# Optimization experiments

Hardware: AMD Instinct MI355X
Metric: run time of the kernel (lower is better)

## Reference

```python
import jax, jax.numpy as jnp
import numpy as np
from jax import lax

D = 768          # embed_dim
H = 12           # n_heads
DEPTH = 2
T = 6            # n_timepoints
PS = 7           # patch_size
IMG = (56, 49, 49)
GRID = (8, 7, 7)
NPATCH = 392     # prod(GRID), must be even for the sinusoidal PE
SEQ = T * NPATCH # 2352 space-time tokens
MLP_H = 3072     # int(768 * 4.0)
B = 2
RRELU_MLP = 0.4        # eval-mode RReLU(0.1, 0.7) slope
RRELU_HEAD = 11.0/48.0 # eval-mode RReLU(1/8, 1/3) slope


def _ln(x, g, b, eps=1e-6):
    m = x.mean(-1, keepdims=True)
    v = ((x - m) ** 2).mean(-1, keepdims=True)
    return (x - m) / jnp.sqrt(v + eps) * g + b


def _pos_enc(t, d):
    pos = np.arange(t, dtype=np.float32)[:, None]
    div = 1.0 / 10000.0 ** (np.arange(0, d, 2, dtype=np.float32) / d)
    pe = np.zeros((t, d), np.float32)
    pe[:, 0::2] = np.sin(pos * div)
    pe[:, 1::2] = np.cos(pos * div)
    return jnp.asarray(pe)


def _convT_dw(x, w, bias, stride, dilation):
    # depthwise ConvTranspose3d(C, C, k, stride, dilation, groups=C); w: (C,1,k,k,k)
    C = x.shape[1]
    k = w.shape[-1]
    wf = jnp.flip(w, axis=(2, 3, 4))
    pad = (k - 1) * dilation
    y = lax.conv_general_dilated(
        x, wf, window_strides=(1, 1, 1), padding=[(pad, pad)] * 3,
        lhs_dilation=(stride,) * 3, rhs_dilation=(dilation,) * 3,
        dimension_numbers=('NCDHW', 'OIDHW', 'NCDHW'), feature_group_count=C)
    return y + bias[None, :, None, None, None]


def _nearest(x, size):
    # torch F.interpolate(mode='nearest'): src = floor(dst * in/out)
    for ax, s in zip((2, 3, 4), size):
        idx = (jnp.arange(s) * (x.shape[ax] / s)).astype(jnp.int32)
        x = jnp.take(x, idx, axis=ax)
    return x


def setup_inputs() -> dict:
    key = jax.random.key(0)
    ks = iter(jax.random.split(key, 64))
    def rn(shape, s=0.02):
        return jax.random.normal(next(ks), shape, jnp.float32) * s
    inp = {}
    inp['x'] = jax.random.normal(next(ks), (B, 1, T) + IMG, jnp.float32)
    inp['pconv_w'] = rn((D, 1, PS, PS, PS)); inp['pconv_b'] = rn((D,))
    inp['pos_embed'] = rn((1, SEQ, D))
    inp['ln1_g'] = jnp.ones((DEPTH, D)); inp['ln1_b'] = jnp.zeros((DEPTH, D))
    inp['qkv_w'] = rn((DEPTH, 3 * D, D)); inp['qkv_b'] = rn((DEPTH, 3 * D))
    inp['proj_w'] = rn((DEPTH, D, D)); inp['proj_b'] = rn((DEPTH, D))
    inp['ln2_g'] = jnp.ones((DEPTH, D)); inp['ln2_b'] = jnp.zeros((DEPTH, D))
    inp['fc1_w'] = rn((DEPTH, MLP_H, D)); inp['fc1_b'] = rn((DEPTH, MLP_H))
    inp['fc2_w'] = rn((DEPTH, D, MLP_H)); inp['fc2_b'] = rn((DEPTH, D))
    inp['normf_g'] = jnp.ones((D,)); inp['normf_b'] = jnp.zeros((D,))
    inp['dfc_w'] = rn((1, D)); inp['dfc_b'] = rn((1,))
    inp['up1_w'] = rn((T, 1, 7, 7, 7)); inp['up1_b'] = rn((T,))
    inp['up2_w'] = rn((T, 1, 5, 5, 5)); inp['up2_b'] = rn((T,))
    inp['up3_w'] = rn((T, 1, 9, 9, 9)); inp['up3_b'] = rn((T,))
    inp['hconv_w'] = rn((T, 1, 1, 1, 1)); inp['hconv_b'] = rn((T,))
    return inp


def reference(x, pconv_w, pconv_b, pos_embed, ln1_g, ln1_b, qkv_w, qkv_b,
              proj_w, proj_b, ln2_g, ln2_b, fc1_w, fc1_b, fc2_w, fc2_b,
              normf_g, normf_b, dfc_w, dfc_b, up1_w, up1_b, up2_w, up2_b,
              up3_w, up3_b, hconv_w, hconv_b):
    b = x.shape[0]
    hd = D // H
    scale = hd ** -0.5
    # fold time into batch, patch-embed each 3D frame
    xt = x.transpose(0, 2, 1, 3, 4, 5).reshape(b * T, 1, *IMG)
    y = lax.conv_general_dilated(
        xt, pconv_w, (PS, PS, PS), 'VALID',
        dimension_numbers=('NCDHW', 'OIDHW', 'NCDHW'))
    y = y + pconv_b[None, :, None, None, None]
    tok = y.reshape(b * T, D, NPATCH).transpose(0, 2, 1).reshape(b, SEQ, D)
    tok = tok + pos_embed
    for i in range(DEPTH):
        h = _ln(tok, ln1_g[i], ln1_b[i])
        qkv = (h @ qkv_w[i].T + qkv_b[i]).reshape(b, SEQ, 3, H, hd)
        qkv = qkv.transpose(2, 0, 3, 1, 4)  # (3,b,H,SEQ,hd)
        q, k, v = qkv[0], qkv[1], qkv[2]
        attn = jax.nn.softmax(jnp.einsum('bhnd,bhmd->bhnm', q, k) * scale, axis=-1)
        o = jnp.einsum('bhnm,bhmd->bhnd', attn, v)
        o = o.transpose(0, 2, 1, 3).reshape(b, SEQ, D)
        tok = tok + (o @ proj_w[i].T + proj_b[i])
        h = _ln(tok, ln2_g[i], ln2_b[i])
        h = h @ fc1_w[i].T + fc1_b[i]
        h = jnp.where(h >= 0, h, RRELU_MLP * h)
        tok = tok + (h @ fc2_w[i].T + fc2_b[i])
    tok = _ln(tok, normf_g, normf_b)
    z = tok.reshape(b, T, NPATCH, D)
    # --- DecoderHead ---
    z = (z @ dfc_w.T + dfc_b)[..., 0]           # (b,T,NPATCH)
    z = z - z.mean(axis=1, keepdims=True)       # subtract time mean
    z = z + _pos_enc(T, NPATCH)
    z = z.reshape(b, T, *GRID)                  # (b,T,8,7,7)
    z = _convT_dw(z, up1_w, up1_b, 1, 1)        # -> (b,T,14,13,13)
    z = _convT_dw(z, up2_w, up2_b, 2, 1)        # -> (b,T,31,29,29)
    z = _convT_dw(z, up3_w, up3_b, 1, 2)        # -> (b,T,47,45,45)
    z = _nearest(z, IMG)                        # -> (b,T,56,49,49)
    z = z * hconv_w[:, 0, 0, 0, 0][None, :, None, None, None] \
        + hconv_b[None, :, None, None, None]
    z = jnp.where(z >= 0, z, RRELU_HEAD * z)
    return z[:, None].transpose(0, 1, 3, 4, 5, 2)  # (b,1,56,49,49,T)
```

## Files before the change

### kernel.cpp

```cpp
#include <hip/hip_runtime.h>


#define AS1 __attribute__((address_space(1)))
#define AS3 __attribute__((address_space(3)))

using bf16 = __bf16;
typedef __bf16 bf16x8 __attribute__((ext_vector_type(8)));
typedef float  f32x4  __attribute__((ext_vector_type(4)));

#define CDIV(a, b) (((a) + (b) - 1) / (b))

__device__ __forceinline__ void gll16(const void* g, void* l) {
  __builtin_amdgcn_global_load_lds((AS1 void*)(void*)g, (AS3 void*)l, 16, 0, 0);
}

template <int SH>
__device__ __forceinline__ float rorf(float x) {
  int i = __builtin_amdgcn_update_dpp(0, __builtin_bit_cast(int, x),
                                      0x120 + SH, 0xF, 0xF, false);
  return __builtin_bit_cast(float, i);
}
__device__ __forceinline__ float rowsum16(float v) {
  v += rorf<1>(v); v += rorf<2>(v); v += rorf<4>(v); v += rorf<8>(v);
  return v;
}

__global__ __launch_bounds__(256) void gemm_bt(
    const bf16* __restrict__ A, const bf16* __restrict__ B,
    float* Cf, bf16* Cb, const float* __restrict__ bias,
    const float* addp, int addmod, int rrelu,
    int M, int N, int K, int lda, int ldb, int ldc,
    long long sA, long long sB, long long sC, int ksplit,
    bf16* __restrict__ Qo, bf16* __restrict__ Ko, bf16* __restrict__ Vo) {
  __shared__ __align__(16) bf16 As[128 * 32];
  __shared__ __align__(16) bf16 Bs[128 * 32];
  const int tid  = threadIdx.x;
  const int lane = tid & 63;
  const int wave = tid >> 6;
  const int wm = wave & 1;
  const int wn = wave >> 1;
  const int q  = lane >> 4;
  const int r  = lane & 15;
  const int tm0 = blockIdx.x * 128;
  const int tn0 = blockIdx.y * 128;
  const int z   = blockIdx.z;

  const bf16* Ab = A + (ksplit > 1 ? 0 : (size_t)z * (size_t)sA);
  const bf16* Bb = B + (ksplit > 1 ? 0 : (size_t)z * (size_t)sB);
  int kb = 0, ke = K;
  if (ksplit > 1) {
    const int kc = ((K / ksplit + 31) / 32) * 32;
    kb = z * kc;
    ke = min(kb + kc, K);
  }

  const int arow0 = min(tm0 + (tid >> 2), M - 1);
  const int arow1 = min(tm0 + (tid >> 2) + 64, M - 1);
  const int brow0 = min(tn0 + (tid >> 2), N - 1);
  const int brow1 = min(tn0 + (tid >> 2) + 64, N - 1);
  const int kcol  = (tid & 3) * 8;
  const bf16* ap0 = Ab + (size_t)arow0 * lda + kcol;
  const bf16* ap1 = Ab + (size_t)arow1 * lda + kcol;
  const bf16* bp0 = Bb + (size_t)brow0 * ldb + kcol;
  const bf16* bp1 = Bb + (size_t)brow1 * ldb + kcol;
  bf16* asw0 = &As[(wave * 64) * 8];
  bf16* asw1 = &As[(256 + wave * 64) * 8];
  bf16* bsw0 = &Bs[(wave * 64) * 8];
  bf16* bsw1 = &Bs[(256 + wave * 64) * 8];

  f32x4 acc[4][4];
#pragma unroll
  for (int mi = 0; mi < 4; ++mi)
#pragma unroll
    for (int ni = 0; ni < 4; ++ni) acc[mi][ni] = (f32x4){0.f, 0.f, 0.f, 0.f};

  for (int k0 = kb; k0 < ke; k0 += 32) {
    __syncthreads();
    gll16(ap0 + k0, asw0);
    gll16(ap1 + k0, asw1);
    gll16(bp0 + k0, bsw0);
    gll16(bp1 + k0, bsw1);
    __syncthreads();
    bf16x8 af[4], bfr[4];
#pragma unroll
    for (int mi = 0; mi < 4; ++mi)
      af[mi] = *(const bf16x8*)&As[(wm * 64 + mi * 16 + r) * 32 + q * 8];
#pragma unroll
    for (int ni = 0; ni < 4; ++ni)
      bfr[ni] = *(const bf16x8*)&Bs[(wn * 64 + ni * 16 + r) * 32 + q * 8];
#pragma unroll
    for (int mi = 0; mi < 4; ++mi)
#pragma unroll
      for (int ni = 0; ni < 4; ++ni)
        acc[mi][ni] = __builtin_amdgcn_mfma_f32_16x16x32_bf16(
            af[mi], bfr[ni], acc[mi][ni], 0, 0, 0);
  }

  float* cf = Cf ? Cf + (ksplit > 1 ? 0 : (size_t)z * (size_t)sC) : nullptr;
  bf16*  cb = Cb ? Cb + (ksplit > 1 ? 0 : (size_t)z * (size_t)sC) : nullptr;
#pragma unroll
  for (int mi = 0; mi < 4; ++mi) {
    const int row0 = tm0 + wm * 64 + mi * 16 + q * 4;
#pragma unroll
    for (int ni = 0; ni < 4; ++ni) {
      const int col = tn0 + wn * 64 + ni * 16 + r;
      if (col >= N) continue;
      const float bv = bias ? bias[col] : 0.f;
#pragma unroll
      for (int reg = 0; reg < 4; ++reg) {
        const int rr = row0 + reg;
        if (rr >= M) continue;
        if (Qo) {
          const float v = acc[mi][ni][reg] + bv;
          const int which = col / 768;
          const int hh = (col % 768) >> 6;
          const int dd = col & 63;
          const int bb2 = rr / 2352;
          const int ss = rr - bb2 * 2352;
          const int inst = bb2 * 12 + hh;
          if (which == 0)
            Qo[((size_t)inst * 2432 + ss) * 64 + dd] = (bf16)v;
          else if (which == 1)
            Ko[((size_t)inst * 2368 + ss) * 64 + dd] = (bf16)(v * 0.18033688f);
          else
            Vo[((size_t)inst * 64 + dd) * 2368 + ss] = (bf16)v;
        } else if (ksplit > 1) {
          float v = acc[mi][ni][reg];
          if (z == 0) {
            v += bv;
            if (addp) v += addp[(size_t)(rr % addmod) * ldc + col];
          }
          atomicAdd(&cf[(size_t)rr * ldc + col], v);
        } else {
          float v = acc[mi][ni][reg] + bv;
          if (addp) v += addp[(size_t)(rr % addmod) * ldc + col];
          if (rrelu) v = (v >= 0.f) ? v : 0.4f * v;
          if (cf) cf[(size_t)rr * ldc + col] = v;
          else    cb[(size_t)rr * ldc + col] = (bf16)v;
        }
      }
    }
  }
}

__global__ __launch_bounds__(256) void flash_attn_split(
    const bf16* __restrict__ Qg, const bf16* __restrict__ Kg,
    const bf16* __restrict__ Vt, float* __restrict__ Opart,
    float* __restrict__ Lpart) {
  __shared__ __align__(16) bf16 Plds[4][2][16 * 72];
  const int lane = threadIdx.x & 63;
  const int wave = threadIdx.x >> 6;
  const int q = lane >> 4, r = lane & 15;
  const int inst = blockIdx.y;
  const int z = blockIdx.z;
  const int rt = blockIdx.x * 4 + wave;
  if (rt >= 74) return;
  const int row0 = rt * 32;
  const int ch0 = (z * 37) >> 1;
  const int ch1 = ((z + 1) * 37) >> 1;
  const bf16* Qi = Qg + (size_t)inst * 2432 * 64;
  const bf16* Ki = Kg + (size_t)inst * 2368 * 64;
  const bf16* Vi = Vt + (size_t)inst * 64 * 2368;

  bf16x8 qf[2][2];
#pragma unroll
  for (int t = 0; t < 2; ++t) {
    qf[t][0] = *(const bf16x8*)&Qi[(size_t)(row0 + t * 16 + r) * 64 + q * 8];
    qf[t][1] = *(const bf16x8*)&Qi[(size_t)(row0 + t * 16 + r) * 64 + 32 + q * 8];
  }

  f32x4 O[2][4];
  float l[2][4];
#pragma unroll
  for (int t = 0; t < 2; ++t)
#pragma unroll
    for (int i = 0; i < 4; ++i) {
      O[t][i] = (f32x4){0.f, 0.f, 0.f, 0.f};
      l[t][i] = 0.f;
    }

  bf16x8 kf0[4], kf1[4];
#pragma unroll
  for (int ct = 0; ct < 4; ++ct) {
    const bf16* kp = &Ki[(size_t)(ch0 * 64 + ct * 16 + r) * 64 + q * 8];
    kf0[ct] = *(const bf16x8*)kp;
    kf1[ct] = *(const bf16x8*)(kp + 32);
  }

  for (int ch = ch0; ch < ch1; ++ch) {
    const int col0 = ch * 64;
    bf16x8 vf0[4], vf1[4];
#pragma unroll
    for (int ot = 0; ot < 4; ++ot) {
      const bf16* vp = &Vi[(size_t)(ot * 16 + r) * 2368 + col0 + q * 8];
      vf0[ot] = *(const bf16x8*)vp;
      vf1[ot] = *(const bf16x8*)(vp + 32);
    }
    f32x4 s[2][4];
#pragma unroll
    for (int ct = 0; ct < 4; ++ct) {
#pragma unroll
      for (int t = 0; t < 2; ++t) {
        f32x4 a = (f32x4){0.f, 0.f, 0.f, 0.f};
        a = __builtin_amdgcn_mfma_f32_16x16x32_bf16(qf[t][0], kf0[ct], a, 0, 0, 0);
        a = __builtin_amdgcn_mfma_f32_16x16x32_bf16(qf[t][1], kf1[ct], a, 0, 0, 0);
        s[t][ct] = a;
      }
    }
    if (ch == 36) {
      s[0][3] = (f32x4){-1e30f, -1e30f, -1e30f, -1e30f};
      s[1][3] = (f32x4){-1e30f, -1e30f, -1e30f, -1e30f};
    }
    const int chn = (ch + 1 < 37) ? ch + 1 : 36;
#pragma unroll
    for (int ct = 0; ct < 4; ++ct) {
      const bf16* kp = &Ki[(size_t)(chn * 64 + ct * 16 + r) * 64 + q * 8];
      kf0[ct] = *(const bf16x8*)kp;
      kf1[ct] = *(const bf16x8*)(kp + 32);
    }
#pragma unroll
    for (int t = 0; t < 2; ++t) {
      float csum[4] = {0.f, 0.f, 0.f, 0.f};
#pragma unroll
      for (int ct = 0; ct < 4; ++ct)
#pragma unroll
        for (int reg = 0; reg < 4; ++reg) {
          float p = exp2f(s[t][ct][reg]);
          s[t][ct][reg] = p;
          csum[reg] += p;
        }
#pragma unroll
      for (int reg = 0; reg < 4; ++reg)
        l[t][reg] += rowsum16(csum[reg]);
      bf16* Pw = Plds[wave][t];
#pragma unroll
      for (int ct = 0; ct < 4; ++ct)
#pragma unroll
        for (int reg = 0; reg < 4; ++reg)
          Pw[(q * 4 + reg) * 72 + ct * 16 + r] = (bf16)s[t][ct][reg];
    }
#pragma unroll
    for (int t = 0; t < 2; ++t) {
      const bf16* Pw = Plds[wave][t];
      const bf16x8 pf0 = *(const bf16x8*)&Pw[r * 72 + q * 8];
      const bf16x8 pf1 = *(const bf16x8*)&Pw[r * 72 + 32 + q * 8];
#pragma unroll
      for (int ot = 0; ot < 4; ++ot) {
        O[t][ot] = __builtin_amdgcn_mfma_f32_16x16x32_bf16(pf0, vf0[ot], O[t][ot], 0, 0, 0);
        O[t][ot] = __builtin_amdgcn_mfma_f32_16x16x32_bf16(pf1, vf1[ot], O[t][ot], 0, 0, 0);
      }
    }
  }
#pragma unroll
  for (int t = 0; t < 2; ++t) {
    const int p = (z * 24 + inst) * 152 + rt * 2 + t;
    float* Op = Opart + (size_t)p * 1024;
#pragma unroll
    for (int ot = 0; ot < 4; ++ot)
#pragma unroll
      for (int reg = 0; reg < 4; ++reg)
        Op[(q * 4 + reg) * 64 + ot * 16 + r] = O[t][ot][reg];
    if (r == 0) {
#pragma unroll
      for (int reg = 0; reg < 4; ++reg)
        Lpart[(size_t)p * 16 + q * 4 + reg] = l[t][reg];
    }
  }
}

__global__ __launch_bounds__(256) void attn_combine(
    const float* __restrict__ Opart, const float* __restrict__ Lpart,
    bf16* __restrict__ Og) {
  const int tile = blockIdx.x;
  const int inst = blockIdx.y;
  const int bb = inst / 12, hh = inst % 12;
  const int pb = inst * 152 + tile;
#pragma unroll
  for (int i = 0; i < 4; ++i) {
    const int e = threadIdx.x + 256 * i;
    const int row = e >> 6, col = e & 63;
    const float lsum = Lpart[(size_t)pb * 16 + row] +
                       Lpart[(size_t)(3648 + pb) * 16 + row];
    const float osum = Opart[(size_t)pb * 1024 + e] +
                       Opart[(size_t)(3648 + pb) * 1024 + e];
    Og[(size_t)(bb * 2352 + tile * 16 + row) * 768 + hh * 64 + col] =
        (bf16)(osum / lsum);
  }
}


__global__ void zero_pads(bf16* __restrict__ Q, bf16* __restrict__ Kb,
                          bf16* __restrict__ VT) {
  int i = blockIdx.x * 256 + threadIdx.x;
  if (i < 122880) {
    int inst = i / 5120, rem = i % 5120;
    Q[((size_t)inst * 2432 + 2352 + rem / 64) * 64 + (rem & 63)] = (bf16)0.f;
  }
  if (i < 24576) {
    int inst = i / 1024, rem = i % 1024;
    Kb[((size_t)inst * 2368 + 2352 + rem / 64) * 64 + (rem & 63)] = (bf16)0.f;
  }
  if (i < 24576) {
    int inst = i / 1024, rem = i % 1024;
    VT[((size_t)inst * 64 + rem / 16) * 2368 + 2352 + (rem & 15)] = (bf16)0.f;
  }
}

__global__ void cvt_bf16(const float* __restrict__ x, bf16* __restrict__ y, int n) {
  int i = blockIdx.x * 256 + threadIdx.x;
  if (i < n) y[i] = (bf16)x[i];
}

__global__ void prep_pconv(const float* __restrict__ w, bf16* __restrict__ y) {
  int i = blockIdx.x * 256 + threadIdx.x;
  if (i >= 768 * 352) return;
  int d = i / 352, j = i % 352;
  y[i] = (bf16)(j < 343 ? w[d * 343 + j] : 0.f);
}

__global__ void im2col(const float* __restrict__ x, bf16* __restrict__ A) {
  int i = blockIdx.x * 256 + threadIdx.x;
  if (i >= 4704 * 352) return;
  int j = i % 352, tok = i / 352;
  float v = 0.f;
  if (j < 343) {
    int p = tok % 392, bt = tok / 392;
    int kx = j % 7, ky = (j / 7) % 7, kz = j / 49;
    int px = p % 7, py = (p / 7) % 7, pz = p / 49;
    int zz = pz * 7 + kz, yy = py * 7 + ky, xx = px * 7 + kx;
    v = x[(((size_t)bt * 56 + zz) * 49 + yy) * 49 + xx];
  }
  A[i] = (bf16)v;
}

template <typename OT>
__global__ __launch_bounds__(256) void ln_kernel(
    const float* __restrict__ x, const float* __restrict__ g,
    const float* __restrict__ bb, OT* __restrict__ y, int M) {
  int row = blockIdx.x * 4 + (threadIdx.x >> 6);
  int lane = threadIdx.x & 63;
  if (row >= M) return;
  const float* xr = x + (size_t)row * 768;
  float v[12], s = 0.f;
#pragma unroll
  for (int i = 0; i < 12; ++i) { v[i] = xr[lane + i * 64]; s += v[i]; }
#pragma unroll
  for (int off = 32; off; off >>= 1) s += __shfl_xor(s, off, 64);
  float mean = s * (1.f / 768.f);
  float vs = 0.f;
#pragma unroll
  for (int i = 0; i < 12; ++i) { float d = v[i] - mean; vs += d * d; }
#pragma unroll
  for (int off = 32; off; off >>= 1) vs += __shfl_xor(vs, off, 64);
  float inv = 1.f / sqrtf(vs * (1.f / 768.f) + 1e-6f);
#pragma unroll
  for (int i = 0; i < 12; ++i) {
    int j = lane + i * 64;
    y[(size_t)row * 768 + j] = (OT)((v[i] - mean) * inv * g[j] + bb[j]);
  }
}

__global__ __launch_bounds__(256) void dfc_kernel(
    const float* __restrict__ x, const float* __restrict__ w,
    const float* __restrict__ b0, float* __restrict__ z0, int M) {
  int row = blockIdx.x * 4 + (threadIdx.x >> 6);
  int lane = threadIdx.x & 63;
  if (row >= M) return;
  const float* xr = x + (size_t)row * 768;
  float s = 0.f;
#pragma unroll
  for (int i = 0; i < 12; ++i) s += xr[lane + i * 64] * w[lane + i * 64];
#pragma unroll
  for (int off = 32; off; off >>= 1) s += __shfl_xor(s, off, 64);
  if (lane == 0) z0[row] = s + b0[0];
}

__global__ void head_pe(const float* __restrict__ z0, float* __restrict__ z1) {
  int i = blockIdx.x * 256 + threadIdx.x;
  if (i >= 784) return;
  int b = i / 392, p = i % 392;
  float vals[6], m = 0.f;
#pragma unroll
  for (int t = 0; t < 6; ++t) { vals[t] = z0[(b * 6 + t) * 392 + p]; m += vals[t]; }
  m *= (1.f / 6.f);
  float e = (float)(2 * (p >> 1)) / 392.0f;
  float div = powf(10000.f, -e);
#pragma unroll
  for (int t = 0; t < 6; ++t) {
    float arg = (float)t * div;
    float pe = (p & 1) ? cosf(arg) : sinf(arg);
    z1[(b * 6 + t) * 392 + p] = vals[t] - m + pe;
  }
}

template <int ID, int IH, int IW, int PD, int PH, int PWA, int OFF, int ST>
__global__ void pad_in(const float* __restrict__ x, float* __restrict__ Xp) {
  int i = blockIdx.x * 256 + threadIdx.x;
  constexpr int total = 12 * PD * PH * PWA;
  if (i >= total) return;
  int px = i % PWA, t1 = i / PWA;
  int py = t1 % PH, t2 = t1 / PH;
  int pz = t2 % PD, c = t2 / PD;
  float v = 0.f;
  int tz = pz - OFF, ty = py - OFF, tx = px - OFF;
  if (tz >= 0 && ty >= 0 && tx >= 0 &&
      (ST == 1 || (((tz | ty | tx) & 1) == 0))) {
    int iz = tz / ST, iy = ty / ST, ix = tx / ST;
    if (iz < ID && iy < IH && ix < IW)
      v = x[((size_t)(c * ID + iz) * IH + iy) * IW + ix];
  }
  Xp[i] = v;
}

template <int PD, int PH, int PWA, int OD, int OH, int OW, int K, int DIL>
__global__ __launch_bounds__(256) void convt4(
    const float* __restrict__ Xp, const float* __restrict__ w,
    const float* __restrict__ bias, float* __restrict__ y) {
  constexpr int P0  = (K - 1) * DIL;
  constexpr int QX  = (OW + 3) / 4;
  constexpr int NLD = (P0 + 4 + 3) / 4;
  int idx = blockIdx.x * 256 + threadIdx.x;
  if (idx >= OD * OH * QX) return;
  int c = blockIdx.y;
  int qx = idx % QX; int t1 = idx / QX;
  int oy = t1 % OH;  int oz = t1 / OH;
  int ox0 = qx * 4;
  const float* xc = Xp + (size_t)c * (PD * PH * PWA);
  const float* wc = w + (c % 6) * (K * K * K);
  const float bv = bias[c % 6];
  float a0 = bv, a1 = bv, a2 = bv, a3 = bv;
  for (int kz = 0; kz < K; ++kz) {
    const int bz = oz + P0 - kz * DIL;
#pragma unroll
    for (int ky = 0; ky < K; ++ky) {
      const int by = oy + P0 - ky * DIL;
      const float* base = xc + ((size_t)bz * PH + by) * PWA + ox0;
      float buf[NLD * 4];
#pragma unroll
      for (int i = 0; i < NLD; ++i)
        *(f32x4*)&buf[i * 4] = *(const f32x4*)(base + i * 4);
      const float* wr = wc + (kz * K + ky) * K;
#pragma unroll
      for (int kx = 0; kx < K; ++kx) {
        const float wv = wr[kx];
        const int j = P0 - kx * DIL;
        a0 += wv * buf[j + 0];
        a1 += wv * buf[j + 1];
        a2 += wv * buf[j + 2];
        a3 += wv * buf[j + 3];
      }
    }
  }
  float* yp = y + (size_t)c * (OD * OH * OW) + ((size_t)oz * OH + oy) * OW + ox0;
  yp[0] = a0;
  if (ox0 + 1 < OW) yp[1] = a1;
  if (ox0 + 2 < OW) yp[2] = a2;
  if (ox0 + 3 < OW) yp[3] = a3;
}

__global__ void head_final(const float* __restrict__ z4, const float* __restrict__ hw,
                           const float* __restrict__ hb, float* __restrict__ out) {
  int idx = blockIdx.x * 256 + threadIdx.x;
  if (idx >= 1613472) return;
  int t = idx % 6, rdx = idx / 6;
  int xx = rdx % 49; rdx /= 49;
  int yy = rdx % 49; rdx /= 49;
  int zz = rdx % 56; int b = rdx / 56;
  const float rz = (float)(47.0 / 56.0), ry = (float)(45.0 / 49.0);
  int iz = (int)((float)zz * rz);
  int iy = (int)((float)yy * ry);
  int ix = (int)((float)xx * ry);
  float v = z4[(((size_t)(b * 6 + t) * 47 + iz) * 45 + iy) * 45 + ix];
  v = v * hw[t] + hb[t];
  v = (v >= 0.f) ? v : (11.0f / 48.0f) * v;
  out[idx] = v;
}


static inline void launch_gemm(hipStream_t s, const bf16* A, const bf16* B,
                               float* Cf, bf16* Cb, const float* bias,
                               const float* addp, int addmod, int rrelu,
                               int M, int N, int K, int lda, int ldb, int ldc,
                               long long sA, long long sB, long long sC,
                               int nz, int ksplit = 1,
                               bf16* Qo = nullptr, bf16* Ko = nullptr,
                               bf16* Vo = nullptr) {
  dim3 g(CDIV(M, 128), CDIV(N, 128), ksplit > 1 ? ksplit : nz);
  gemm_bt<<<g, 256, 0, s>>>(A, B, Cf, Cb, bias, addp, addmod, rrelu,
                            M, N, K, lda, ldb, ldc, sA, sB, sC, ksplit,
                            Qo, Ko, Vo);
}

extern "C" void kernel_launch(void* const* d_in, const int* in_sizes, int n_in,
                              void* d_out, int out_size, void* d_ws, size_t ws_size,
                              hipStream_t stream) {
  (void)in_sizes; (void)n_in; (void)out_size; (void)ws_size;
  const float* x       = (const float*)d_in[0];
  const float* pconv_w = (const float*)d_in[1];
  const float* pconv_b = (const float*)d_in[2];
  const float* pos_emb = (const float*)d_in[3];
  const float* ln1_g   = (const float*)d_in[4];
  const float* ln1_b   = (const float*)d_in[5];
  const float* qkv_wf  = (const float*)d_in[6];
  const float* qkv_b   = (const float*)d_in[7];
  const float* proj_wf = (const float*)d_in[8];
  const float* proj_b  = (const float*)d_in[9];
  const float* ln2_g   = (const float*)d_in[10];
  const float* ln2_b   = (const float*)d_in[11];
  const float* fc1_wf  = (const float*)d_in[12];
  const float* fc1_b   = (const float*)d_in[13];
  const float* fc2_wf  = (const float*)d_in[14];
  const float* fc2_b   = (const float*)d_in[15];
  const float* normf_g = (const float*)d_in[16];
  const float* normf_b = (const float*)d_in[17];
  const float* dfc_w   = (const float*)d_in[18];
  const float* dfc_b   = (const float*)d_in[19];
  const float* up1_w   = (const float*)d_in[20];
  const float* up1_b   = (const float*)d_in[21];
  const float* up2_w   = (const float*)d_in[22];
  const float* up2_b   = (const float*)d_in[23];
  const float* up3_w   = (const float*)d_in[24];
  const float* up3_b   = (const float*)d_in[25];
  const float* hconv_w = (const float*)d_in[26];
  const float* hconv_b = (const float*)d_in[27];
  float* out = (float*)d_out;

  char* ws = (char*)d_ws;
  size_t off = 0;
  auto alloc = [&](size_t bytes) -> void* {
    void* p = ws + off;
    off += (bytes + 255) & ~(size_t)255;
    return p;
  };
  float* tok   = (float*)alloc(4704UL * 768 * 4);
  bf16* lnout  = (bf16*)alloc(4704UL * 768 * 2);
  bf16* Qb     = (bf16*)alloc(24UL * 2432 * 64 * 2);
  bf16* Kb     = (bf16*)alloc(24UL * 2368 * 64 * 2);
  bf16* VT     = (bf16*)alloc(24UL * 64 * 2368 * 2);
  bf16* attnb  = (bf16*)alloc(4704UL * 768 * 2);
  bf16* hb     = (bf16*)alloc(4704UL * 3072 * 2);
  bf16* Apatch = (bf16*)alloc(4704UL * 352 * 2);
  bf16* Wq     = (bf16*)alloc(2UL * 2304 * 768 * 2);
  bf16* Wp     = (bf16*)alloc(2UL * 768 * 768 * 2);
  bf16* W1     = (bf16*)alloc(2UL * 3072 * 768 * 2);
  bf16* W2     = (bf16*)alloc(2UL * 768 * 3072 * 2);
  bf16* Wpc    = (bf16*)alloc(768UL * 352 * 2);
  float* Opart = (float*)alloc(2UL * 24 * 152 * 1024 * 4);
  float* Lpart = (float*)alloc(2UL * 24 * 152 * 16 * 4);
  float* z0    = (float*)alloc(4704UL * 4);
  float* z1    = (float*)alloc(4704UL * 4);
  float* z2    = (float*)alloc(12UL * 14 * 13 * 13 * 4);
  float* z3    = (float*)alloc(12UL * 31 * 29 * 29 * 4);
  float* z4    = (float*)alloc(12UL * 47 * 45 * 45 * 4);
  float* p1    = (float*)alloc(12UL * 20 * 19 * 24 * 4);
  float* p2    = (float*)alloc(12UL * 35 * 33 * 36 * 4);
  float* p3    = (float*)alloc(12UL * 63 * 61 * 64 * 4);
  float* lnf   = (float*)alloc(4704UL * 768 * 4);

  cvt_bf16<<<CDIV(3538944, 256), 256, 0, stream>>>(qkv_wf, Wq, 3538944);
  cvt_bf16<<<CDIV(1179648, 256), 256, 0, stream>>>(proj_wf, Wp, 1179648);
  cvt_bf16<<<CDIV(4718592, 256), 256, 0, stream>>>(fc1_wf, W1, 4718592);
  cvt_bf16<<<CDIV(4718592, 256), 256, 0, stream>>>(fc2_wf, W2, 4718592);
  prep_pconv<<<CDIV(768 * 352, 256), 256, 0, stream>>>(pconv_w, Wpc);
  zero_pads<<<CDIV(122880, 256), 256, 0, stream>>>(Qb, Kb, VT);

  im2col<<<CDIV(4704 * 352, 256), 256, 0, stream>>>(x, Apatch);
  launch_gemm(stream, Apatch, Wpc, tok, nullptr, pconv_b, pos_emb, 2352, 0,
              4704, 768, 352, 352, 352, 768, 0, 0, 0, 1);

  for (int i = 0; i < 2; ++i) {
    ln_kernel<bf16><<<1176, 256, 0, stream>>>(tok, ln1_g + i * 768, ln1_b + i * 768, lnout, 4704);
    launch_gemm(stream, lnout, Wq + (size_t)i * 2304 * 768, nullptr, nullptr,
                qkv_b + i * 2304, nullptr, 1, 0,
                4704, 2304, 768, 768, 768, 2304, 0, 0, 0, 1, 1, Qb, Kb, VT);
    flash_attn_split<<<dim3(19, 24, 2), 256, 0, stream>>>(Qb, Kb, VT, Opart, Lpart);
    attn_combine<<<dim3(147, 24), 256, 0, stream>>>(Opart, Lpart, attnb);
    launch_gemm(stream, attnb, Wp + (size_t)i * 768 * 768, tok, nullptr,
                proj_b + i * 768, nullptr, 1, 0,
                4704, 768, 768, 768, 768, 768, 0, 0, 0, 1, 4);
    ln_kernel<bf16><<<1176, 256, 0, stream>>>(tok, ln2_g + i * 768, ln2_b + i * 768, lnout, 4704);
    launch_gemm(stream, lnout, W1 + (size_t)i * 3072 * 768, nullptr, hb,
                fc1_b + i * 3072, nullptr, 1, 1,
                4704, 3072, 768, 768, 768, 3072, 0, 0, 0, 1);
    launch_gemm(stream, hb, W2 + (size_t)i * 768 * 3072, tok, nullptr,
                fc2_b + i * 768, nullptr, 1, 0,
                4704, 768, 3072, 3072, 3072, 768, 0, 0, 0, 1, 4);
  }

  ln_kernel<float><<<1176, 256, 0, stream>>>(tok, normf_g, normf_b, lnf, 4704);
  dfc_kernel<<<1176, 256, 0, stream>>>(lnf, dfc_w, dfc_b, z0, 4704);
  head_pe<<<4, 256, 0, stream>>>(z0, z1);

  pad_in<8, 7, 7, 20, 19, 24, 6, 1>
      <<<CDIV(12 * 20 * 19 * 24, 256), 256, 0, stream>>>(z1, p1);
  convt4<20, 19, 24, 14, 13, 13, 7, 1>
      <<<dim3(CDIV(14 * 13 * 4, 256), 12), 256, 0, stream>>>(p1, up1_w, up1_b, z2);
  pad_in<14, 13, 13, 35, 33, 36, 4, 2>
      <<<CDIV(12 * 35 * 33 * 36, 256), 256, 0, stream>>>(z2, p2);
  convt4<35, 33, 36, 31, 29, 29, 5, 1>
      <<<dim3(CDIV(31 * 29 * 8, 256), 12), 256, 0, stream>>>(p2, up2_w, up2_b, z3);
  pad_in<31, 29, 29, 63, 61, 64, 16, 1>
      <<<CDIV(12 * 63 * 61 * 64, 256), 256, 0, stream>>>(z3, p3);
  convt4<63, 61, 64, 47, 45, 45, 9, 2>
      <<<dim3(CDIV(47 * 45 * 12, 256), 12), 256, 0, stream>>>(p3, up3_w, up3_b, z4);

  head_final<<<CDIV(1613472, 256), 256, 0, stream>>>(z4, hconv_w, hconv_b, out);
}
```

Before: 1.182 ms.

## Share K/V tiles across waves via LDS in split flash attention

After: 1.086 ms. -8.1%, faster.

```diff
diff --git a/kernel.cpp b/kernel.cpp
--- a/kernel.cpp
+++ b/kernel.cpp
@@ -147,14 +147,16 @@
     const bf16* __restrict__ Qg, const bf16* __restrict__ Kg,
     const bf16* __restrict__ Vt, float* __restrict__ Opart,
     float* __restrict__ Lpart) {
+  __shared__ __align__(16) bf16 Kl[64 * 64];
+  __shared__ __align__(16) bf16 Vl[64 * 64];
   __shared__ __align__(16) bf16 Plds[4][2][16 * 72];
   const int lane = threadIdx.x & 63;
   const int wave = threadIdx.x >> 6;
   const int q = lane >> 4, r = lane & 15;
   const int inst = blockIdx.y;
   const int z = blockIdx.z;
-  const int rt = blockIdx.x * 4 + wave;
-  if (rt >= 74) return;
+  const int rt_raw = blockIdx.x * 4 + wave;
+  const int rt = min(rt_raw, 73);
   const int row0 = rt * 32;
   const int ch0 = (z * 37) >> 1;
   const int ch1 = ((z + 1) * 37) >> 1;
@@ -179,23 +181,33 @@
       l[t][i] = 0.f;
     }
 
-  bf16x8 kf0[4], kf1[4];
-#pragma unroll
-  for (int ct = 0; ct < 4; ++ct) {
-    const bf16* kp = &Ki[(size_t)(ch0 * 64 + ct * 16 + r) * 64 + q * 8];
-    kf0[ct] = *(const bf16x8*)kp;
-    kf1[ct] = *(const bf16x8*)(kp + 32);
-  }
+  const int rl = lane >> 3;
+  const int ul = lane & 7;
+  const int swz = (r & 7);
 
   for (int ch = ch0; ch < ch1; ++ch) {
     const int col0 = ch * 64;
-    bf16x8 vf0[4], vf1[4];
-#pragma unroll
-    for (int ot = 0; ot < 4; ++ot) {
-      const bf16* vp = &Vi[(size_t)(ot * 16 + r) * 2368 + col0 + q * 8];
-      vf0[ot] = *(const bf16x8*)vp;
-      vf1[ot] = *(const bf16x8*)(vp + 32);
-    }
+    __syncthreads();
+#pragma unroll
+    for (int j = 0; j < 2; ++j) {
+      const int g = wave * 2 + j;
+      const int row = g * 8 + rl;
+      const int ug = ul ^ (row & 7);
+      gll16(Ki + ((size_t)(col0 + row) * 64 + ug * 8), &Kl[g * 512]);
+      gll16(Vi + (size_t)row * 2368 + col0 + ug * 8, &Vl[g * 512]);
+    }
+    __syncthreads();
+
+    bf16x8 kf0[4], kf1[4], vf0[4], vf1[4];
+#pragma unroll
+    for (int ct = 0; ct < 4; ++ct) {
+      const int krow = ct * 16 + r;
+      kf0[ct] = *(const bf16x8*)&Kl[krow * 64 + ((q ^ swz) * 8)];
+      kf1[ct] = *(const bf16x8*)&Kl[krow * 64 + (((q + 4) ^ swz) * 8)];
+      vf0[ct] = *(const bf16x8*)&Vl[krow * 64 + ((q ^ swz) * 8)];
+      vf1[ct] = *(const bf16x8*)&Vl[krow * 64 + (((q + 4) ^ swz) * 8)];
+    }
+
     f32x4 s[2][4];
 #pragma unroll
     for (int ct = 0; ct < 4; ++ct) {
@@ -211,13 +223,6 @@
       s[0][3] = (f32x4){-1e30f, -1e30f, -1e30f, -1e30f};
       s[1][3] = (f32x4){-1e30f, -1e30f, -1e30f, -1e30f};
     }
-    const int chn = (ch + 1 < 37) ? ch + 1 : 36;
-#pragma unroll
-    for (int ct = 0; ct < 4; ++ct) {
-      const bf16* kp = &Ki[(size_t)(chn * 64 + ct * 16 + r) * 64 + q * 8];
-      kf0[ct] = *(const bf16x8*)kp;
-      kf1[ct] = *(const bf16x8*)(kp + 32);
-    }
 #pragma unroll
     for (int t = 0; t < 2; ++t) {
       float csum[4] = {0.f, 0.f, 0.f, 0.f};
@@ -251,19 +256,21 @@
       }
     }
   }
-#pragma unroll
-  for (int t = 0; t < 2; ++t) {
-    const int p = (z * 24 + inst) * 152 + rt * 2 + t;
-    float* Op = Opart + (size_t)p * 1024;
-#pragma unroll
-    for (int ot = 0; ot < 4; ++ot)
-#pragma unroll
-      for (int reg = 0; reg < 4; ++reg)
-        Op[(q * 4 + reg) * 64 + ot * 16 + r] = O[t][ot][reg];
-    if (r == 0) {
-#pragma unroll
-      for (int reg = 0; reg < 4; ++reg)
-        Lpart[(size_t)p * 16 + q * 4 + reg] = l[t][reg];
+  if (rt_raw < 74) {
+#pragma unroll
+    for (int t = 0; t < 2; ++t) {
+      const int p = (z * 24 + inst) * 152 + rt * 2 + t;
+      float* Op = Opart + (size_t)p * 1024;
+#pragma unroll
+      for (int ot = 0; ot < 4; ++ot)
+#pragma unroll
+        for (int reg = 0; reg < 4; ++reg)
+          Op[(q * 4 + reg) * 64 + ot * 16 + r] = O[t][ot][reg];
+      if (r == 0) {
+#pragma unroll
+        for (int reg = 0; reg < 4; ++reg)
+          Lpart[(size_t)p * 16 + q * 4 + reg] = l[t][reg];
+      }
     }
   }
 }
```
